# Optimization experiments

Measured on AMD Instinct MI355X. Metric: run time of the kernel, lower is better.

Reference implementation:

```python
import jax, jax.numpy as jnp
import numpy as np

NUM_HEADS = 16


def setup_inputs() -> dict:
    key = jax.random.key(0)
    ks = jax.random.split(key, 4)
    B, C, T, D = 1, 1, 3072, 1024
    s = 1.0 / np.sqrt(D)
    return {
        "x": jax.random.normal(ks[0], (B, C, T, D), dtype=jnp.float32),
        "Wq": jax.random.normal(ks[1], (D, D), dtype=jnp.float32) * s,
        "bq": jnp.zeros((D,), dtype=jnp.float32),
        "Wk": jax.random.normal(ks[2], (D, D), dtype=jnp.float32) * s,
        "bk": jnp.zeros((D,), dtype=jnp.float32),
        "Wv": jax.random.normal(ks[3], (D, D), dtype=jnp.float32) * s,
        "bv": jnp.zeros((D,), dtype=jnp.float32),
        "gamma": jnp.float32(0.5),  # learned scalar; 0.0 at torch init, nonzero here for a meaningful signal
    }


def reference(x, Wq, bq, Wk, bk, Wv, bv, gamma):
    # x: (B, C, T, D); Linear acts on last dim (torch: y = x @ W.T + b)
    B, C, T, D = x.shape
    H = NUM_HEADS
    q = (jnp.einsum("bctd,ed->bcte", x, Wq) + bq).reshape(B, -1, T, H)  # (B, X, T, H), X = C*D/H
    k = (jnp.einsum("bctd,ed->bcte", x, Wk) + bk).reshape(B, -1, T, H)
    v = (jnp.einsum("bctd,ed->bcte", x, Wv) + bv).reshape(B, -1, T, H)
    q = q.transpose(0, 3, 2, 1)  # (B, H, T, X)
    k = k.transpose(0, 3, 1, 2)  # (B, H, X, T)
    energy = q @ k               # (B, H, T, T)  -- note: NO 1/sqrt(d) scaling, as in source
    attn = jax.nn.softmax(energy, axis=-1)
    v = v.transpose(0, 3, 2, 1)  # (B, H, T, X)
    out = attn @ v               # (B, H, T, X)
    out = out.transpose(0, 2, 3, 1).reshape(B, T, -1)  # (B, T, X*H) = (B, T, C*D)
    # residual broadcast: (B, T, C*D) + (B, C, T, D); valid since B == C == 1
    return gamma * out + x
```

## Files before the change

kernel.cpp:

```cpp
#include <hip/hip_runtime.h>


typedef _Float16 v8h __attribute__((ext_vector_type(8)));
typedef _Float16 v4h __attribute__((ext_vector_type(4)));
typedef __fp16   v2pk __attribute__((ext_vector_type(2)));
typedef __fp16   v4pk __attribute__((ext_vector_type(4)));
typedef float    v4f __attribute__((ext_vector_type(4)));

#define TSEQ 3072
#define DM   1024
#define NH   16
#define XD   64
#define LOG2E 1.44269504f

__device__ __forceinline__ void async_load16(const void* g, void* l) {
  __builtin_amdgcn_global_load_lds(
      (const __attribute__((address_space(1))) unsigned int*)g,
      (__attribute__((address_space(3))) unsigned int*)l,
      16, 0, 0);
}

__device__ __forceinline__ float fexp2(float x) {
  float r; asm("v_exp_f32 %0, %1" : "=v"(r) : "v"(x)); return r;
}
__device__ __forceinline__ float flog2(float x) {
  float r; asm("v_log_f32 %0, %1" : "=v"(r) : "v"(x)); return r;
}
__device__ __forceinline__ float fmax3(float a, float b, float c) {
  return fmaxf(fmaxf(a, b), c);
}

extern "C" __global__ __launch_bounds__(256) void cvt_kernel(
    const float* __restrict__ x, const float* __restrict__ wq,
    const float* __restrict__ wk, const float* __restrict__ wv,
    _Float16* __restrict__ xb, _Float16* __restrict__ wb)
{
  const int NX4 = (TSEQ * DM) / 4;
  const int NT  = NX4 * 2;
  for (int i = blockIdx.x * blockDim.x + threadIdx.x; i < NT;
       i += gridDim.x * blockDim.x) {
    float4 v;
    _Float16* dst;
    if (i < NX4) {
      v = ((const float4*)x)[i];
      dst = xb + (size_t)i * 4;
    } else {
      const int j = i - NX4;
      const int n = j >> 8;
      if (n < 1024)      v = ((const float4*)wq)[j];
      else if (n < 2048) v = ((const float4*)wk)[j - 262144];
      else               v = ((const float4*)wv)[j - 524288];
      dst = wb + (size_t)j * 4;
    }
    v4h h;
    h[0] = (_Float16)v.x; h[1] = (_Float16)v.y;
    h[2] = (_Float16)v.z; h[3] = (_Float16)v.w;
    *(v4h*)dst = h;
  }
}

extern "C" __global__ __launch_bounds__(256) void qkv_gemm_kernel(
    const _Float16* __restrict__ xb, const _Float16* __restrict__ wb,
    const float* __restrict__ bq, const float* __restrict__ bk,
    const float* __restrict__ bv,
    _Float16* __restrict__ qlin, _Float16* __restrict__ klin,
    _Float16* __restrict__ vlin)
{
  __shared__ _Float16 As[128 * 32];
  __shared__ _Float16 Bs[128 * 32];
  const int tid = threadIdx.x;
  const int w = tid >> 6, l = tid & 63;
  const int li = l & 15, lg = l >> 4;
  const int wm = w >> 1, wn = w & 1;
  const int bid = blockIdx.x;
  const int swz = (bid & 7) * 72 + (bid >> 3);
  const int m0 = (swz / 24) * 128, n0 = (swz % 24) * 128;
  v4f acc[4][4] = {};
  const int srow = l >> 2;
  const int scol = (l & 3) * 8;
  for (int k0 = 0; k0 < DM; k0 += 32) {
#pragma unroll
    for (int c = 0; c < 2; ++c) {
      const int rbase = c * 64 + w * 16;
      async_load16(xb + (size_t)(m0 + rbase + srow) * DM + k0 + scol, &As[rbase * 32]);
      async_load16(wb + (size_t)(n0 + rbase + srow) * DM + k0 + scol, &Bs[rbase * 32]);
    }
    __syncthreads();
    v8h af[4], bf[4];
#pragma unroll
    for (int mi = 0; mi < 4; ++mi)
      af[mi] = *(const v8h*)&As[(wm * 64 + mi * 16 + li) * 32 + lg * 8];
#pragma unroll
    for (int ni = 0; ni < 4; ++ni)
      bf[ni] = *(const v8h*)&Bs[(wn * 64 + ni * 16 + li) * 32 + lg * 8];
#pragma unroll
    for (int mi = 0; mi < 4; ++mi)
#pragma unroll
      for (int ni = 0; ni < 4; ++ni)
        acc[mi][ni] = __builtin_amdgcn_mfma_f32_16x16x32_f16(
            af[mi], bf[ni], acc[mi][ni], 0, 0, 0);
    __syncthreads();
  }
  const int which = n0 >> 10;
  const int ebase = n0 & 1023;
  const float* bias = which == 0 ? bq : (which == 1 ? bk : bv);
  _Float16* outp = which == 0 ? qlin : (which == 1 ? klin : vlin);
#pragma unroll
  for (int mi = 0; mi < 4; ++mi)
#pragma unroll
    for (int r = 0; r < 4; ++r) {
      const int t = m0 + wm * 64 + mi * 16 + lg * 4 + r;
#pragma unroll
      for (int ni = 0; ni < 4; ++ni) {
        const int e = ebase + wn * 64 + ni * 16 + li;
        outp[(size_t)t * DM + e] = (_Float16)(acc[mi][ni][r] + bias[e]);
      }
    }
}

extern "C" __global__ __launch_bounds__(256) void repack_kernel(
    const _Float16* __restrict__ qlin, const _Float16* __restrict__ klin,
    const _Float16* __restrict__ vlin,
    _Float16* __restrict__ qh, _Float16* __restrict__ kh,
    _Float16* __restrict__ vt)
{
  const int NE = NH * TSEQ * XD;
  for (int g = blockIdx.x * blockDim.x + threadIdx.x; g < 3 * NE;
       g += gridDim.x * blockDim.x) {
    if (g < 2 * NE) {
      const int gg = (g < NE) ? g : g - NE;
      const int xx = gg & 63;
      const int rest = gg >> 6;
      const int h = rest / TSEQ;
      const int i = rest - h * TSEQ;
      const int t = xx * 48 + (i >> 6);
      const int e = ((i & 63) << 4) + h;
      if (g < NE) qh[gg] = qlin[t * DM + e];
      else        kh[gg] = (_Float16)((float)klin[t * DM + e] * LOG2E);
    } else {
      const int o = g - 2 * NE;
      const int j = o % TSEQ;
      const int rest = o / TSEQ;
      const int xx = rest & 63;
      const int h = rest >> 6;
      const int t = xx * 48 + (j >> 6);
      const int e = ((j & 63) << 4) + h;
      vt[o] = vlin[t * DM + e];
    }
  }
}

extern "C" __global__ __launch_bounds__(512) void attn_kernel(
    const _Float16* __restrict__ qh, const _Float16* __restrict__ kh,
    const _Float16* __restrict__ vt, _Float16* __restrict__ pOut)
{
  __shared__ _Float16 Ks[2][64 * 64];
  __shared__ _Float16 Vs[2][64 * 64];
  __shared__ float sml[4][16];
  const int tid = threadIdx.x;
  const int w = tid >> 6, l = tid & 63;
  const int li = l & 15, lg = l >> 4;
  const int wq = w & 3, g = w >> 2;
  const int head = blockIdx.y;
  const int i0 = blockIdx.x * 64;
  const size_t hb = (size_t)head * TSEQ * XD;

  v8h qf0, qf1;
  {
    const _Float16* qrow = qh + hb + (size_t)(i0 + wq * 16 + li) * XD;
    qf0 = *(const v8h*)(qrow + lg * 8);
    qf1 = *(const v8h*)(qrow + 32 + lg * 8);
  }
  float m2 = 24.0f * LOG2E;
  float l4 = 0.0f;
  v4f oacc[4] = {};
  const int r8 = l >> 3, c8 = l & 7;

  for (int j0 = 0; j0 < TSEQ; j0 += 128) {
    const int jt = j0 + g * 64;
#pragma unroll
    for (int s = 0; s < 2; ++s) {
      const int n = wq * 2 + s;
      const int row = n * 8 + r8;
      async_load16(kh + hb + (size_t)(jt + row) * XD + ((c8 ^ (row & 7)) * 8),
                   &Ks[g][n * 512]);
      async_load16(vt + hb + (size_t)row * TSEQ + jt + ((c8 ^ (row & 7)) * 8),
                   &Vs[g][n * 512]);
    }
    __syncthreads();

    v4f e4[4];
#pragma unroll
    for (int kt = 0; kt < 4; ++kt) {
      const int krow = kt * 16 + li;
      const v8h kf0 = *(const v8h*)&Ks[g][krow * 64 + ((lg ^ (li & 7)) * 8)];
      const v8h kf1 = *(const v8h*)&Ks[g][krow * 64 + (((4 + lg) ^ (li & 7)) * 8)];
      v4f a = {};
      a = __builtin_amdgcn_mfma_f32_16x16x32_f16(kf0, qf0, a, 0, 0, 0);
      a = __builtin_amdgcn_mfma_f32_16x16x32_f16(kf1, qf1, a, 0, 0, 0);
      e4[kt] = a;
    }

    float p[4][4];
#pragma unroll
    for (int kt = 0; kt < 4; ++kt)
#pragma unroll
      for (int r = 0; r < 4; ++r) p[kt][r] = fexp2(e4[kt][r] - m2);

    const float lmax = fmax3(
        fmax3(fmax3(e4[0][0], e4[0][1], e4[0][2]),
              fmax3(e4[0][3], e4[1][0], e4[1][1]),
              fmax3(e4[1][2], e4[1][3], e4[2][0])),
        fmax3(e4[2][1], e4[2][2], e4[2][3]),
        fmax3(e4[3][0], fmaxf(e4[3][1], e4[3][2]), e4[3][3]));
    if (__any(lmax > m2 + 11.5f)) {
      float rm = lmax;
      rm = fmaxf(rm, __shfl_xor(rm, 16, 64));
      rm = fmaxf(rm, __shfl_xor(rm, 32, 64));
      const float fs = (rm > m2) ? fexp2(m2 - rm) : 1.0f;
#pragma unroll
      for (int kt = 0; kt < 4; ++kt)
#pragma unroll
        for (int r = 0; r < 4; ++r) p[kt][r] *= fs;
      l4 *= fs;
#pragma unroll
      for (int mi = 0; mi < 4; ++mi) oacc[mi] *= fs;
      m2 = fmaxf(m2, rm);
    }

    v4h pv[4];
#pragma unroll
    for (int kt = 0; kt < 4; ++kt) {
      const v2pk lo = __builtin_amdgcn_cvt_pkrtz(p[kt][0], p[kt][1]);
      const v2pk hi = __builtin_amdgcn_cvt_pkrtz(p[kt][2], p[kt][3]);
      const v4pk pk = __builtin_shufflevector(lo, hi, 0, 1, 2, 3);
      pv[kt] = __builtin_bit_cast(v4h, pk);
    }
    l4 += ((p[0][0] + p[0][1]) + (p[0][2] + p[0][3]))
        + ((p[1][0] + p[1][1]) + (p[1][2] + p[1][3]))
        + ((p[2][0] + p[2][1]) + (p[2][2] + p[2][3]))
        + ((p[3][0] + p[3][1]) + (p[3][2] + p[3][3]));

#pragma unroll
    for (int mi = 0; mi < 4; ++mi) {
      const int vrow = mi * 16 + li;
      const int vb = vrow * 64 + (lg & 1) * 4;
      v4f a = oacc[mi];
#pragma unroll
      for (int kt = 0; kt < 4; ++kt) {
        const v4h vf = *(const v4h*)&Vs[g][vb + (((kt * 2 + (lg >> 1)) ^ (li & 7)) * 8)];
        a = __builtin_amdgcn_mfma_f32_16x16x16f16(vf, pv[kt], a, 0, 0, 0);
      }
      oacc[mi] = a;
    }
    __syncthreads();
  }

  float ls = l4;
  ls += __shfl_xor(ls, 16, 64);
  ls += __shfl_xor(ls, 32, 64);
  const float inv = 1.0f / ls;
  const float s = m2 + flog2(ls);
  _Float16* mb = &Ks[0][0];
  if (g == 1) {
    if (lg == 0) sml[wq][li] = s;
#pragma unroll
    for (int mi = 0; mi < 4; ++mi) {
      v4h o4;
#pragma unroll
      for (int r = 0; r < 4; ++r) o4[r] = (_Float16)(oacc[mi][r] * inv);
      *(v4h*)&mb[wq * 1024 + li * 64 + mi * 16 + lg * 4] = o4;
    }
  }
  __syncthreads();
  if (g == 0) {
    const float s1 = sml[wq][li];
    const float M = fmaxf(s, s1);
    const float u0 = fexp2(s - M), u1 = fexp2(s1 - M);
    const float den = 1.0f / (u0 + u1);
    const float c0 = u0 * den * inv, c1 = u1 * den;
    const int irow = i0 + wq * 16 + li;
#pragma unroll
    for (int mi = 0; mi < 4; ++mi) {
      const v4h o1 = *(const v4h*)&mb[wq * 1024 + li * 64 + mi * 16 + lg * 4];
      v4h o4;
#pragma unroll
      for (int r = 0; r < 4; ++r)
        o4[r] = (_Float16)(c0 * oacc[mi][r] + c1 * (float)o1[r]);
      *(v4h*)&pOut[(size_t)irow * DM + head * 64 + mi * 16 + lg * 4] = o4;
    }
  }
}

extern "C" __global__ __launch_bounds__(256) void epilogue_kernel(
    const _Float16* __restrict__ pO, const float* __restrict__ xin,
    const float* __restrict__ gscal, float* __restrict__ outp)
{
  __shared__ _Float16 po[8 * 1024];
  const int tid = threadIdx.x;
  const size_t t0 = (size_t)blockIdx.x * 8;
  {
    const _Float16* src = pO + t0 * DM + tid * 32;
    v8h* d = (v8h*)&po[tid * 32];
#pragma unroll
    for (int c = 0; c < 4; ++c) d[c] = *(const v8h*)(src + c * 8);
  }
  __syncthreads();
  const float g = gscal[0];
  const int tr = tid >> 5;
  const int d0 = (tid & 31) * 32;
  const size_t rb = (t0 + tr) * DM + d0;
#pragma unroll
  for (int c4 = 0; c4 < 8; ++c4) {
    const float4 xi = *(const float4*)&xin[rb + c4 * 4];
    float4 r;
    r.x = g * (float)po[tr * 1024 + ((c4 * 4 + 0) & 15) * 64 + ((d0 + c4 * 4 + 0) >> 4)] + xi.x;
    r.y = g * (float)po[tr * 1024 + ((c4 * 4 + 1) & 15) * 64 + ((d0 + c4 * 4 + 1) >> 4)] + xi.y;
    r.z = g * (float)po[tr * 1024 + ((c4 * 4 + 2) & 15) * 64 + ((d0 + c4 * 4 + 2) >> 4)] + xi.z;
    r.w = g * (float)po[tr * 1024 + ((c4 * 4 + 3) & 15) * 64 + ((d0 + c4 * 4 + 3) >> 4)] + xi.w;
    *(float4*)&outp[rb + c4 * 4] = r;
  }
}

extern "C" void kernel_launch(void* const* d_in, const int* in_sizes, int n_in,
                              void* d_out, int out_size, void* d_ws, size_t ws_size,
                              hipStream_t stream)
{
  const float* x  = (const float*)d_in[0];
  const float* Wq = (const float*)d_in[1];
  const float* bq = (const float*)d_in[2];
  const float* Wk = (const float*)d_in[3];
  const float* bk = (const float*)d_in[4];
  const float* Wv = (const float*)d_in[5];
  const float* bv = (const float*)d_in[6];
  const float* gm = (const float*)d_in[7];
  float* outp = (float*)d_out;
  char* ws = (char*)d_ws;
  const size_t SZH = (size_t)TSEQ * DM * sizeof(_Float16);
  _Float16* xb   = (_Float16*)(ws);
  _Float16* wb   = (_Float16*)(ws + SZH);
  _Float16* qlin = (_Float16*)(ws + 2 * SZH);
  _Float16* klin = (_Float16*)(ws + 3 * SZH);
  _Float16* vlin = (_Float16*)(ws + 4 * SZH);
  _Float16* qhp  = (_Float16*)(ws + 5 * SZH);
  _Float16* khp  = (_Float16*)(ws + 6 * SZH);
  _Float16* vtp  = (_Float16*)(ws + 7 * SZH);
  _Float16* pO   = (_Float16*)(ws);

  cvt_kernel<<<dim3(1024), dim3(256), 0, stream>>>(x, Wq, Wk, Wv, xb, wb);
  qkv_gemm_kernel<<<dim3(576), dim3(256), 0, stream>>>(xb, wb, bq, bk, bv,
                                                       qlin, klin, vlin);
  repack_kernel<<<dim3(4096), dim3(256), 0, stream>>>(qlin, klin, vlin,
                                                      qhp, khp, vtp);
  attn_kernel<<<dim3(48, 16), dim3(512), 0, stream>>>(qhp, khp, vtp, pO);
  epilogue_kernel<<<dim3(384), dim3(256), 0, stream>>>(pO, x, gm, outp);
  (void)in_sizes; (void)n_in; (void)out_size; (void)ws_size;
}
```

Before: 155.0 us.

## Give each attention wave two query tiles to reuse K/V fragments, halve threads

The attention block drops from 8 waves to 4. Each wave now owns 32 query rows (two 16-row tiles), so every K and V fragment read from LDS feeds two MFMAs instead of one, and each thread issues twice as many async loads per tile. The running max is folded into the MFMA accumulator init (-m2) so exp2 is applied directly, and the rescale step subtracts the new max in place. Register pressure roughly doubles and fewer waves per block may reduce latency hiding.

```diff
diff --git a/kernel.cpp b/kernel.cpp
--- a/kernel.cpp
+++ b/kernel.cpp
@@ -25,9 +25,6 @@
 }
 __device__ __forceinline__ float flog2(float x) {
   float r; asm("v_log_f32 %0, %1" : "=v"(r) : "v"(x)); return r;
-}
-__device__ __forceinline__ float fmax3(float a, float b, float c) {
-  return fmaxf(fmaxf(a, b), c);
 }
 
 extern "C" __global__ __launch_bounds__(256) void cvt_kernel(
@@ -150,37 +147,38 @@
   }
 }
 
-extern "C" __global__ __launch_bounds__(512) void attn_kernel(
+extern "C" __global__ __launch_bounds__(256) void attn_kernel(
     const _Float16* __restrict__ qh, const _Float16* __restrict__ kh,
     const _Float16* __restrict__ vt, _Float16* __restrict__ pOut)
 {
-  __shared__ _Float16 Ks[2][64 * 64];
-  __shared__ _Float16 Vs[2][64 * 64];
-  __shared__ float sml[4][16];
+  __shared__ _Float16 Ks[2][4096];
+  __shared__ _Float16 Vs[2][4096];
+  __shared__ float sml[64];
   const int tid = threadIdx.x;
   const int w = tid >> 6, l = tid & 63;
   const int li = l & 15, lg = l >> 4;
-  const int wq = w & 3, g = w >> 2;
+  const int rw = w & 1, g = w >> 1;
   const int head = blockIdx.y;
   const int i0 = blockIdx.x * 64;
   const size_t hb = (size_t)head * TSEQ * XD;
 
-  v8h qf0, qf1;
-  {
-    const _Float16* qrow = qh + hb + (size_t)(i0 + wq * 16 + li) * XD;
-    qf0 = *(const v8h*)(qrow + lg * 8);
-    qf1 = *(const v8h*)(qrow + 32 + lg * 8);
-  }
-  float m2 = 24.0f * LOG2E;
-  float l4 = 0.0f;
-  v4f oacc[4] = {};
+  v8h qf[2][2];
+#pragma unroll
+  for (int ct = 0; ct < 2; ++ct) {
+    const _Float16* qrow = qh + hb + (size_t)(i0 + rw * 32 + ct * 16 + li) * XD;
+    qf[ct][0] = *(const v8h*)(qrow + lg * 8);
+    qf[ct][1] = *(const v8h*)(qrow + 32 + lg * 8);
+  }
+  float m2[2] = {24.0f * LOG2E, 24.0f * LOG2E};
+  float l4[2] = {0.0f, 0.0f};
+  v4f oacc[4][2] = {};
   const int r8 = l >> 3, c8 = l & 7;
 
   for (int j0 = 0; j0 < TSEQ; j0 += 128) {
     const int jt = j0 + g * 64;
 #pragma unroll
-    for (int s = 0; s < 2; ++s) {
-      const int n = wq * 2 + s;
+    for (int s = 0; s < 4; ++s) {
+      const int n = rw * 4 + s;
       const int row = n * 8 + r8;
       async_load16(kh + hb + (size_t)(jt + row) * XD + ((c8 ^ (row & 7)) * 8),
                    &Ks[g][n * 512]);
@@ -189,105 +187,127 @@
     }
     __syncthreads();
 
-    v4f e4[4];
+    v4f e4[2][4];
 #pragma unroll
     for (int kt = 0; kt < 4; ++kt) {
       const int krow = kt * 16 + li;
       const v8h kf0 = *(const v8h*)&Ks[g][krow * 64 + ((lg ^ (li & 7)) * 8)];
       const v8h kf1 = *(const v8h*)&Ks[g][krow * 64 + (((4 + lg) ^ (li & 7)) * 8)];
-      v4f a = {};
-      a = __builtin_amdgcn_mfma_f32_16x16x32_f16(kf0, qf0, a, 0, 0, 0);
-      a = __builtin_amdgcn_mfma_f32_16x16x32_f16(kf1, qf1, a, 0, 0, 0);
-      e4[kt] = a;
-    }
-
-    float p[4][4];
-#pragma unroll
-    for (int kt = 0; kt < 4; ++kt)
-#pragma unroll
-      for (int r = 0; r < 4; ++r) p[kt][r] = fexp2(e4[kt][r] - m2);
-
-    const float lmax = fmax3(
-        fmax3(fmax3(e4[0][0], e4[0][1], e4[0][2]),
-              fmax3(e4[0][3], e4[1][0], e4[1][1]),
-              fmax3(e4[1][2], e4[1][3], e4[2][0])),
-        fmax3(e4[2][1], e4[2][2], e4[2][3]),
-        fmax3(e4[3][0], fmaxf(e4[3][1], e4[3][2]), e4[3][3]));
-    if (__any(lmax > m2 + 11.5f)) {
-      float rm = lmax;
-      rm = fmaxf(rm, __shfl_xor(rm, 16, 64));
-      rm = fmaxf(rm, __shfl_xor(rm, 32, 64));
-      const float fs = (rm > m2) ? fexp2(m2 - rm) : 1.0f;
+#pragma unroll
+      for (int ct = 0; ct < 2; ++ct) {
+        v4f a = {-m2[ct], -m2[ct], -m2[ct], -m2[ct]};
+        a = __builtin_amdgcn_mfma_f32_16x16x32_f16(kf0, qf[ct][0], a, 0, 0, 0);
+        a = __builtin_amdgcn_mfma_f32_16x16x32_f16(kf1, qf[ct][1], a, 0, 0, 0);
+        e4[ct][kt] = a;
+      }
+    }
+
+    float gm = -1.0e30f;
+#pragma unroll
+    for (int ct = 0; ct < 2; ++ct)
 #pragma unroll
       for (int kt = 0; kt < 4; ++kt)
-#pragma unroll
-        for (int r = 0; r < 4; ++r) p[kt][r] *= fs;
-      l4 *= fs;
-#pragma unroll
-      for (int mi = 0; mi < 4; ++mi) oacc[mi] *= fs;
-      m2 = fmaxf(m2, rm);
-    }
-
-    v4h pv[4];
-#pragma unroll
-    for (int kt = 0; kt < 4; ++kt) {
-      const v2pk lo = __builtin_amdgcn_cvt_pkrtz(p[kt][0], p[kt][1]);
-      const v2pk hi = __builtin_amdgcn_cvt_pkrtz(p[kt][2], p[kt][3]);
-      const v4pk pk = __builtin_shufflevector(lo, hi, 0, 1, 2, 3);
-      pv[kt] = __builtin_bit_cast(v4h, pk);
-    }
-    l4 += ((p[0][0] + p[0][1]) + (p[0][2] + p[0][3]))
-        + ((p[1][0] + p[1][1]) + (p[1][2] + p[1][3]))
-        + ((p[2][0] + p[2][1]) + (p[2][2] + p[2][3]))
-        + ((p[3][0] + p[3][1]) + (p[3][2] + p[3][3]));
+        gm = fmaxf(fmaxf(gm, fmaxf(e4[ct][kt][0], e4[ct][kt][1])),
+                   fmaxf(e4[ct][kt][2], e4[ct][kt][3]));
+    if (__any(gm > 11.5f)) {
+#pragma unroll
+      for (int ct = 0; ct < 2; ++ct) {
+        float rm = -1.0e30f;
+#pragma unroll
+        for (int kt = 0; kt < 4; ++kt)
+          rm = fmaxf(fmaxf(rm, fmaxf(e4[ct][kt][0], e4[ct][kt][1])),
+                     fmaxf(e4[ct][kt][2], e4[ct][kt][3]));
+        rm = fmaxf(rm, __shfl_xor(rm, 16, 64));
+        rm = fmaxf(rm, __shfl_xor(rm, 32, 64));
+        rm = fmaxf(rm, 0.0f);
+        const float fs = fexp2(-rm);
+#pragma unroll
+        for (int kt = 0; kt < 4; ++kt)
+#pragma unroll
+          for (int r = 0; r < 4; ++r) e4[ct][kt][r] -= rm;
+        l4[ct] *= fs;
+#pragma unroll
+        for (int mi = 0; mi < 4; ++mi) oacc[mi][ct] *= fs;
+        m2[ct] += rm;
+      }
+    }
+
+    v4h pv[2][4];
+#pragma unroll
+    for (int ct = 0; ct < 2; ++ct) {
+#pragma unroll
+      for (int kt = 0; kt < 4; ++kt) {
+        const float p0 = fexp2(e4[ct][kt][0]);
+        const float p1 = fexp2(e4[ct][kt][1]);
+        const float p2 = fexp2(e4[ct][kt][2]);
+        const float p3 = fexp2(e4[ct][kt][3]);
+        const v2pk lo = __builtin_amdgcn_cvt_pkrtz(p0, p1);
+        const v2pk hi = __builtin_amdgcn_cvt_pkrtz(p2, p3);
+        const v4pk pk = __builtin_shufflevector(lo, hi, 0, 1, 2, 3);
+        pv[ct][kt] = __builtin_bit_cast(v4h, pk);
+        l4[ct] += (p0 + p1) + (p2 + p3);
+      }
+    }
 
 #pragma unroll
     for (int mi = 0; mi < 4; ++mi) {
       const int vrow = mi * 16 + li;
       const int vb = vrow * 64 + (lg & 1) * 4;
-      v4f a = oacc[mi];
 #pragma unroll
       for (int kt = 0; kt < 4; ++kt) {
         const v4h vf = *(const v4h*)&Vs[g][vb + (((kt * 2 + (lg >> 1)) ^ (li & 7)) * 8)];
-        a = __builtin_amdgcn_mfma_f32_16x16x16f16(vf, pv[kt], a, 0, 0, 0);
-      }
-      oacc[mi] = a;
+#pragma unroll
+        for (int ct = 0; ct < 2; ++ct)
+          oacc[mi][ct] = __builtin_amdgcn_mfma_f32_16x16x16f16(
+              vf, pv[ct][kt], oacc[mi][ct], 0, 0, 0);
+      }
     }
     __syncthreads();
   }
 
-  float ls = l4;
-  ls += __shfl_xor(ls, 16, 64);
-  ls += __shfl_xor(ls, 32, 64);
-  const float inv = 1.0f / ls;
-  const float s = m2 + flog2(ls);
+  float sv[2], inv[2];
+#pragma unroll
+  for (int ct = 0; ct < 2; ++ct) {
+    float ls = l4[ct];
+    ls += __shfl_xor(ls, 16, 64);
+    ls += __shfl_xor(ls, 32, 64);
+    inv[ct] = 1.0f / ls;
+    sv[ct] = m2[ct] + flog2(ls);
+  }
   _Float16* mb = &Ks[0][0];
   if (g == 1) {
-    if (lg == 0) sml[wq][li] = s;
-#pragma unroll
-    for (int mi = 0; mi < 4; ++mi) {
-      v4h o4;
-#pragma unroll
-      for (int r = 0; r < 4; ++r) o4[r] = (_Float16)(oacc[mi][r] * inv);
-      *(v4h*)&mb[wq * 1024 + li * 64 + mi * 16 + lg * 4] = o4;
+#pragma unroll
+    for (int ct = 0; ct < 2; ++ct) {
+      const int rl = rw * 32 + ct * 16 + li;
+      if (lg == 0) sml[rl] = sv[ct];
+#pragma unroll
+      for (int mi = 0; mi < 4; ++mi) {
+        v4h o4;
+#pragma unroll
+        for (int r = 0; r < 4; ++r) o4[r] = (_Float16)(oacc[mi][ct][r] * inv[ct]);
+        *(v4h*)&mb[rl * 64 + mi * 16 + lg * 4] = o4;
+      }
     }
   }
   __syncthreads();
   if (g == 0) {
-    const float s1 = sml[wq][li];
-    const float M = fmaxf(s, s1);
-    const float u0 = fexp2(s - M), u1 = fexp2(s1 - M);
-    const float den = 1.0f / (u0 + u1);
-    const float c0 = u0 * den * inv, c1 = u1 * den;
-    const int irow = i0 + wq * 16 + li;
-#pragma unroll
-    for (int mi = 0; mi < 4; ++mi) {
-      const v4h o1 = *(const v4h*)&mb[wq * 1024 + li * 64 + mi * 16 + lg * 4];
-      v4h o4;
-#pragma unroll
-      for (int r = 0; r < 4; ++r)
-        o4[r] = (_Float16)(c0 * oacc[mi][r] + c1 * (float)o1[r]);
-      *(v4h*)&pOut[(size_t)irow * DM + head * 64 + mi * 16 + lg * 4] = o4;
+#pragma unroll
+    for (int ct = 0; ct < 2; ++ct) {
+      const int rl = rw * 32 + ct * 16 + li;
+      const float s1 = sml[rl];
+      const float M = fmaxf(sv[ct], s1);
+      const float u0 = fexp2(sv[ct] - M), u1 = fexp2(s1 - M);
+      const float den = 1.0f / (u0 + u1);
+      const float c0 = u0 * den * inv[ct], c1 = u1 * den;
+#pragma unroll
+      for (int mi = 0; mi < 4; ++mi) {
+        const v4h o1 = *(const v4h*)&mb[rl * 64 + mi * 16 + lg * 4];
+        v4h o4;
+#pragma unroll
+        for (int r = 0; r < 4; ++r)
+          o4[r] = (_Float16)(c0 * oacc[mi][ct][r] + c1 * (float)o1[r]);
+        *(v4h*)&pOut[(size_t)(i0 + rl) * DM + head * 64 + mi * 16 + lg * 4] = o4;
+      }
     }
   }
 }
@@ -352,7 +372,7 @@
                                                        qlin, klin, vlin);
   repack_kernel<<<dim3(4096), dim3(256), 0, stream>>>(qlin, klin, vlin,
                                                       qhp, khp, vtp);
-  attn_kernel<<<dim3(48, 16), dim3(512), 0, stream>>>(qhp, khp, vtp, pO);
+  attn_kernel<<<dim3(48, 16), dim3(256), 0, stream>>>(qhp, khp, vtp, pO);
   epilogue_kernel<<<dim3(384), dim3(256), 0, stream>>>(pO, x, gm, outp);
   (void)in_sizes; (void)n_in; (void)out_size; (void)ws_size;
 }
```

Result: no change. 155.6 us (+0.4%).
